# Performance work log

Measured on AMD Instinct MI355X. Metric: run time of the kernel, lower is better.

The kernel has to match this reference:

```python
import jax, jax.numpy as jnp
import numpy as np

EPS = 1e-5
D_STATE = 16
D_INNER = 2
D_CONV = 4


def batchnorm(x, g, b):
    # BatchNorm1d in training mode: biased batch statistics over the batch dim
    m = x.mean(axis=0)
    v = x.var(axis=0)
    return g * (x - m) * jax.lax.rsqrt(v + EPS) + b


def mamba(u, W_in, conv_w, conv_b, W_xproj, W_dt, b_dt, A_log, D, W_out):
    # u: [B, L, 1] (d_model=1, d_inner=2, d_state=16, dt_rank=1)
    Bsz, L, _ = u.shape
    xz = jnp.einsum('bld,ed->ble', u, W_in)            # [B,L,4]
    x, z = jnp.split(xz, 2, axis=-1)                    # [B,L,2] each
    # causal depthwise conv along L
    xc = jnp.transpose(x, (0, 2, 1))                    # [B,C,L]
    xc = jax.lax.conv_general_dilated(
        xc, conv_w, (1,), [(D_CONV - 1, 0)],
        dimension_numbers=('NCH', 'OIH', 'NCH'),
        feature_group_count=D_INNER)
    x = jax.nn.silu(jnp.transpose(xc, (0, 2, 1)) + conv_b)  # [B,L,2]
    x_dbl = jnp.einsum('ble,fe->blf', x, W_xproj)       # [B,L,1+2*16]
    dt = jax.nn.softplus(jnp.einsum('blr,er->ble', x_dbl[..., :1], W_dt) + b_dt)  # [B,L,2]
    Bm = x_dbl[..., 1:1 + D_STATE]                      # [B,L,16]
    Cm = x_dbl[..., 1 + D_STATE:1 + 2 * D_STATE]        # [B,L,16]
    A = -jnp.exp(A_log)                                 # [2,16]

    def step(h, inp):
        dt_t, B_t, C_t, x_t = inp                       # [B,2],[B,16],[B,16],[B,2]
        dA = jnp.exp(dt_t[:, :, None] * A)              # [B,2,16]
        h = h * dA + dt_t[:, :, None] * B_t[:, None, :] * x_t[:, :, None]
        y = jnp.einsum('ben,bn->be', h, C_t) + D * x_t
        return h, y

    h0 = jnp.zeros((Bsz, D_INNER, D_STATE), u.dtype)
    xs = (dt.transpose(1, 0, 2), Bm.transpose(1, 0, 2),
          Cm.transpose(1, 0, 2), x.transpose(1, 0, 2))
    _, ys = jax.lax.scan(step, h0, xs)                  # [L,B,2]
    y = ys.transpose(1, 0, 2) * jax.nn.silu(z)          # [B,L,2]
    return jnp.einsum('ble,de->bld', y, W_out)          # [B,L,1]


def setup_inputs() -> dict:
    key = jax.random.key(0)
    ks = jax.random.split(key, 16)
    B = 1024
    s = 0.02
    inp = {
        'x': jax.random.normal(ks[0], (B, 1775), jnp.float32),
        'W1': jax.random.normal(ks[1], (2048, 1775), jnp.float32) * s,
        'g1': jnp.ones((2048,), jnp.float32),
        'b1': jnp.zeros((2048,), jnp.float32),
        'W_in': jax.random.normal(ks[2], (2 * D_INNER, 1), jnp.float32) * s,
        'conv_w': jax.random.normal(ks[3], (D_INNER, 1, D_CONV), jnp.float32) * 0.2,
        'conv_b': jnp.zeros((D_INNER,), jnp.float32),
        'W_xproj': jax.random.normal(ks[4], (1 + 2 * D_STATE, D_INNER), jnp.float32) * 0.2,
        'W_dt': jax.random.normal(ks[5], (D_INNER, 1), jnp.float32) * 0.2,
        'b_dt': jax.random.normal(ks[6], (D_INNER,), jnp.float32) * 0.2,
        'A_log': jnp.tile(jnp.log(jnp.arange(1, D_STATE + 1, dtype=jnp.float32)), (D_INNER, 1)),
        'D': jnp.ones((D_INNER,), jnp.float32),
        'W_out': jax.random.normal(ks[7], (1, D_INNER), jnp.float32) * 0.2,
        'W2': jax.random.normal(ks[8], (512, 2048), jnp.float32) * s,
        'g2': jnp.ones((512,), jnp.float32),
        'b2': jnp.zeros((512,), jnp.float32),
        'W3': jax.random.normal(ks[9], (256, 512), jnp.float32) * s,
    }
    return inp


def reference(x, W1, g1, b1, W_in, conv_w, conv_b, W_xproj, W_dt, b_dt,
              A_log, D, W_out, W2, g2, b2, W3):
    h = batchnorm(x @ W1.T, g1, b1)                     # [B,2048]
    h = mamba(h[:, :, None], W_in, conv_w, conv_b, W_xproj, W_dt, b_dt,
              A_log, D, W_out)[:, :, 0]                 # [B,2048]
    h = jax.nn.relu(batchnorm(h @ W2.T, g2, b2))        # [B,512]
    return h @ W3.T                                     # [B,256]
```

## Files before the change

kernel.cpp:

```cpp
#include <hip/hip_runtime.h>
#include <math.h>

#define SEQL 2048
#define BATCH 1024
#define CHUNK 128
#define NCH 16

typedef _Float16 f16x8 __attribute__((ext_vector_type(8)));
typedef _Float16 f16x4 __attribute__((ext_vector_type(4)));
typedef _Float16 h2 __attribute__((ext_vector_type(2)));
typedef float f32x4 __attribute__((ext_vector_type(4)));

__device__ inline unsigned short f2h(float f) {
    _Float16 h = (_Float16)f;
    return *reinterpret_cast<unsigned short*>(&h);
}
__device__ inline float packh2(float a, float b) {
    return __uint_as_float((unsigned)f2h(a) | ((unsigned)f2h(b) << 16));
}
__device__ inline float hext(float packed, int sh) {
    const unsigned short s = (unsigned short)(__float_as_uint(packed) >> sh);
    _Float16 h = *reinterpret_cast<const _Float16*>(&s);
    return (float)h;
}

__device__ inline void gl2lds16(const void* g, void* l) {
    __builtin_amdgcn_global_load_lds(
        (const __attribute__((address_space(1))) unsigned int*)g,
        (__attribute__((address_space(3))) unsigned int*)l, 16, 0, 0);
}

template<int CTRL>
__device__ inline float dppadd(float v) {
    const int p = __builtin_amdgcn_update_dpp(0, __float_as_int(v), CTRL, 0xF, 0xF, true);
    return v + __int_as_float(p);
}

__global__ __launch_bounds__(256) void cvt_all(
    const float* __restrict__ x, const float* __restrict__ W1,
    const float* __restrict__ W2, const float* __restrict__ W3,
    _Float16* __restrict__ xh, _Float16* __restrict__ w1h,
    _Float16* __restrict__ w2h, _Float16* __restrict__ w3h)
{
    const int bid = blockIdx.x;
    if (bid < 3072) {
        const float* src; _Float16* dst;
        if (bid < 1024) { src = x + (size_t)bid * 1775;           dst = xh  + (size_t)bid * 1792; }
        else            { src = W1 + (size_t)(bid - 1024) * 1775; dst = w1h + (size_t)(bid - 1024) * 1792; }
        f16x4* dst4 = reinterpret_cast<f16x4*>(dst);
        for (int i = threadIdx.x; i < 448; i += 256) {
            const int k = i * 4;
            float4 v = {0.f, 0.f, 0.f, 0.f};
            if (k + 3 < 1775) v = *reinterpret_cast<const float4*>(&src[k]);
            else {
                if (k     < 1775) v.x = src[k];
                if (k + 1 < 1775) v.y = src[k + 1];
                if (k + 2 < 1775) v.z = src[k + 2];
            }
            f16x4 o; o[0] = (_Float16)v.x; o[1] = (_Float16)v.y; o[2] = (_Float16)v.z; o[3] = (_Float16)v.w;
            dst4[i] = o;
        }
    } else {
        const float* src; _Float16* dst; int nvec;
        if (bid < 3584) { const int r = bid - 3072; src = W2 + (size_t)r * 2048; dst = w2h + (size_t)r * 2048; nvec = 512; }
        else            { const int r = bid - 3584; src = W3 + (size_t)r * 512;  dst = w3h + (size_t)r * 512;  nvec = 128; }
        f16x4* dst4 = reinterpret_cast<f16x4*>(dst);
        for (int i = threadIdx.x; i < nvec; i += 256) {
            const float4 v = reinterpret_cast<const float4*>(src)[i];
            f16x4 o; o[0] = (_Float16)v.x; o[1] = (_Float16)v.y; o[2] = (_Float16)v.z; o[3] = (_Float16)v.w;
            dst4[i] = o;
        }
    }
}

__global__ __launch_bounds__(256) void cvt_bnrelu(
    const float* __restrict__ P0, const float* __restrict__ P1,
    const float* __restrict__ sc, const float* __restrict__ tc,
    _Float16* __restrict__ h3)
{
    const int row = blockIdx.x * 2 + (threadIdx.x >> 7);
    const int i = threadIdx.x & 127;
    const float4 p0 = reinterpret_cast<const float4*>(P0 + (size_t)row * 512)[i];
    const float4 p1 = reinterpret_cast<const float4*>(P1 + (size_t)row * 512)[i];
    const float4 sv = reinterpret_cast<const float4*>(sc)[i];
    const float4 tv = reinterpret_cast<const float4*>(tc)[i];
    f16x4 o;
    o[0] = (_Float16)fmaxf(fmaf(sv.x, p0.x + p1.x, tv.x), 0.f);
    o[1] = (_Float16)fmaxf(fmaf(sv.y, p0.y + p1.y, tv.y), 0.f);
    o[2] = (_Float16)fmaxf(fmaf(sv.z, p0.z + p1.z, tv.z), 0.f);
    o[3] = (_Float16)fmaxf(fmaf(sv.w, p0.w + p1.w, tv.w), 0.f);
    reinterpret_cast<f16x4*>(h3 + (size_t)row * 512)[i] = o;
}

__global__ __launch_bounds__(256) void gemm_f16(
    const _Float16* __restrict__ A, const _Float16* __restrict__ B,
    float* __restrict__ C, int ldc, int Kp, int ksteps, size_t coff,
    float* __restrict__ bnp, int bn_ld)
{
    __shared__ __attribute__((aligned(16))) _Float16 sA[64 * 64];
    __shared__ __attribute__((aligned(16))) _Float16 sB[64 * 64];

    const int tid = threadIdx.x;
    const int wave = tid >> 6;
    const int lane = tid & 63;
    const int m0 = blockIdx.y * 64;
    const int n0 = blockIdx.x * 64;
    C += (size_t)blockIdx.z * coff;

    const int srow = tid >> 3;
    const int pslot = tid & 7;
    const int gslot = pslot ^ (srow & 7);
    const size_t gk0 = (size_t)blockIdx.z * ksteps * 64 + gslot * 8;
    const _Float16* gA0 = A + (size_t)(m0 + srow) * Kp + gk0;
    const _Float16* gA1 = A + (size_t)(m0 + 32 + srow) * Kp + gk0;
    const _Float16* gB0 = B + (size_t)(n0 + srow) * Kp + gk0;
    const _Float16* gB1 = B + (size_t)(n0 + 32 + srow) * Kp + gk0;
    const int wdst = wave * 512;

    const int wr = wave >> 1, wc = wave & 1;
    const int li = lane & 15, gq = lane >> 4;
    const int p0s = (gq    ) ^ (li & 7);
    const int p1s = (gq + 4) ^ (li & 7);

    f32x4 acc[2][2];
    #pragma unroll
    for (int i = 0; i < 2; ++i)
        #pragma unroll
        for (int j = 0; j < 2; ++j)
            #pragma unroll
            for (int v = 0; v < 4; ++v) acc[i][j][v] = 0.f;

    for (int kt = 0; kt < ksteps; ++kt) {
        const size_t go = (size_t)kt * 64;
        gl2lds16(gA0 + go, &sA[wdst]);
        gl2lds16(gA1 + go, &sA[2048 + wdst]);
        gl2lds16(gB0 + go, &sB[wdst]);
        gl2lds16(gB1 + go, &sB[2048 + wdst]);
        __syncthreads();

        f16x8 af[2][2], bg[2][2];
        #pragma unroll
        for (int mi = 0; mi < 2; ++mi) {
            const int rb = (wr * 32 + mi * 16 + li) * 64;
            af[mi][0] = *(const f16x8*)&sA[rb + p0s * 8];
            af[mi][1] = *(const f16x8*)&sA[rb + p1s * 8];
        }
        #pragma unroll
        for (int ni = 0; ni < 2; ++ni) {
            const int rb = (wc * 32 + ni * 16 + li) * 64;
            bg[ni][0] = *(const f16x8*)&sB[rb + p0s * 8];
            bg[ni][1] = *(const f16x8*)&sB[rb + p1s * 8];
        }
        #pragma unroll
        for (int mi = 0; mi < 2; ++mi)
            #pragma unroll
            for (int ni = 0; ni < 2; ++ni) {
                acc[mi][ni] = __builtin_amdgcn_mfma_f32_16x16x32_f16(af[mi][0], bg[ni][0], acc[mi][ni], 0, 0, 0);
                acc[mi][ni] = __builtin_amdgcn_mfma_f32_16x16x32_f16(af[mi][1], bg[ni][1], acc[mi][ni], 0, 0, 0);
            }
        __syncthreads();
    }

    #pragma unroll
    for (int mi = 0; mi < 2; ++mi)
        #pragma unroll
        for (int ni = 0; ni < 2; ++ni) {
            const int col = n0 + wc * 32 + ni * 16 + li;
            #pragma unroll
            for (int i = 0; i < 4; ++i) {
                const int row = m0 + wr * 32 + mi * 16 + gq * 4 + i;
                C[(size_t)row * ldc + col] = acc[mi][ni][i];
            }
        }

    if (bnp) {
        #pragma unroll
        for (int ni = 0; ni < 2; ++ni) {
            float ps = 0.f, pq = 0.f;
            #pragma unroll
            for (int mi = 0; mi < 2; ++mi)
                #pragma unroll
                for (int i = 0; i < 4; ++i) {
                    const float v = acc[mi][ni][i];
                    ps += v; pq += v * v;
                }
            ps += __shfl_xor(ps, 16); ps += __shfl_xor(ps, 32);
            pq += __shfl_xor(pq, 16); pq += __shfl_xor(pq, 32);
            if (gq == 0) {
                const int col = n0 + wc * 32 + ni * 16 + li;
                const int grp = blockIdx.y * 2 + wr;
                bnp[(size_t)(grp * 2    ) * bn_ld + col] = ps;
                bnp[(size_t)(grp * 2 + 1) * bn_ld + col] = pq;
            }
        }
    }
}

__global__ __launch_bounds__(256) void bn_part(
    const float* __restrict__ X, const float* __restrict__ X2,
    int rows_per, int ld, float* __restrict__ part)
{
    __shared__ float rs[4][64], rq[4][64];
    const int tid = threadIdx.x;
    const int c = tid & 63, rg4 = tid >> 6;
    const int col = blockIdx.x * 64 + c;
    const int r0 = blockIdx.y * rows_per;
    float sum = 0.f, sq = 0.f;
    for (int r = rg4; r < rows_per; r += 4) {
        const size_t idx = (size_t)(r0 + r) * ld + col;
        float v = X[idx];
        if (X2) v += X2[idx];
        sum += v; sq += v * v;
    }
    rs[rg4][c] = sum; rq[rg4][c] = sq;
    __syncthreads();
    if (rg4 == 0) {
        sum = rs[0][c] + rs[1][c] + rs[2][c] + rs[3][c];
        sq  = rq[0][c] + rq[1][c] + rq[2][c] + rq[3][c];
        part[((size_t)blockIdx.y * 2    ) * ld + col] = sum;
        part[((size_t)blockIdx.y * 2 + 1) * ld + col] = sq;
    }
}

__global__ __launch_bounds__(256) void bn_fin(
    const float* __restrict__ part, int RG, int ld, float inv_rows,
    const float* __restrict__ g, const float* __restrict__ b,
    float* __restrict__ s, float* __restrict__ t)
{
    const int col = blockIdx.x * 256 + threadIdx.x;
    if (col >= ld) return;
    float sum = 0.f, sq = 0.f;
    for (int z = 0; z < RG; ++z) {
        sum += part[((size_t)z * 2    ) * ld + col];
        sq  += part[((size_t)z * 2 + 1) * ld + col];
    }
    const float mean = sum * inv_rows;
    const float var = fmaxf(sq * inv_rows - mean * mean, 0.f);
    const float rstd = 1.0f / sqrtf(var + 1e-5f);
    const float sv = g[col] * rstd;
    s[col] = sv;
    t[col] = b[col] - mean * sv;
}

__global__ __launch_bounds__(512, 8) void mamba_scan7(
    const float* __restrict__ Y, _Float16* __restrict__ a2,
    const float* __restrict__ s1, const float* __restrict__ t1,
    const float* __restrict__ Win, const float* __restrict__ convw,
    const float* __restrict__ convb, const float* __restrict__ Wx,
    const float* __restrict__ Wdt, const float* __restrict__ bdt,
    const float* __restrict__ Alog, const float* __restrict__ Dp,
    const float* __restrict__ Wout)
{
    __shared__ __align__(16) float4 pk[SEQL];
    __shared__ float Ps[NCH][32];
    __shared__ float Ss[NCH][32];
    __shared__ float Hin[NCH][32];

    const int tid = threadIdx.x;
    const int row = blockIdx.x;
    const float* yrow = Y + (size_t)row * SEQL;
    _Float16* a2row = a2 + (size_t)row * SEQL;

    {
        const int l0 = tid * 4;
        float4 ym = {0.f,0.f,0.f,0.f}, sm = {0.f,0.f,0.f,0.f}, tm = {0.f,0.f,0.f,0.f};
        if (tid > 0) {
            ym = *reinterpret_cast<const float4*>(&yrow[l0 - 4]);
            sm = *reinterpret_cast<const float4*>(&s1[l0 - 4]);
            tm = *reinterpret_cast<const float4*>(&t1[l0 - 4]);
        }
        const float4 y0 = *reinterpret_cast<const float4*>(&yrow[l0]);
        const float4 s0 = *reinterpret_cast<const float4*>(&s1[l0]);
        const float4 t0 = *reinterpret_cast<const float4*>(&t1[l0]);

        float ua[8];
        ua[0] = fmaf(sm.x, ym.x, tm.x);
        ua[1] = fmaf(sm.y, ym.y, tm.y);
        ua[2] = fmaf(sm.z, ym.z, tm.z);
        ua[3] = fmaf(sm.w, ym.w, tm.w);
        ua[4] = fmaf(s0.x, y0.x, t0.x);
        ua[5] = fmaf(s0.y, y0.y, t0.y);
        ua[6] = fmaf(s0.z, y0.z, t0.z);
        ua[7] = fmaf(s0.w, y0.w, t0.w);

        const float wi0 = Win[0], wi1 = Win[1];
        const float wz0 = Win[2], wz1 = Win[3];
        const float wo0 = Wout[0], wo1 = Wout[1];
        const float cw00 = convw[0], cw01 = convw[1], cw02 = convw[2], cw03 = convw[3];
        const float cw10 = convw[4], cw11 = convw[5], cw12 = convw[6], cw13 = convw[7];
        const float cb0 = convb[0], cb1 = convb[1];
        const float wx00 = Wx[0], wx01 = Wx[1];
        const float wdt0 = Wdt[0], wdt1 = Wdt[1];
        const float bdt0 = bdt[0], bdt1 = bdt[1];

        #pragma unroll
        for (int j = 0; j < 4; ++j) {
            const float u0 = ua[j + 4], um1 = ua[j + 3], um2 = ua[j + 2], um3 = ua[j + 1];
            const float c0 = fmaf(wi0, cw00 * um3 + cw01 * um2 + cw02 * um1 + cw03 * u0, cb0);
            const float c1 = fmaf(wi1, cw10 * um3 + cw11 * um2 + cw12 * um1 + cw13 * u0, cb1);
            const float xs0 = c0 / (1.f + __expf(-c0));
            const float xs1 = c1 / (1.f + __expf(-c1));
            const float d0 = xs0 * wx00 + xs1 * wx01;
            const float dt0 = __logf(1.f + __expf(fmaf(d0, wdt0, bdt0)));
            const float dt1 = __logf(1.f + __expf(fmaf(d0, wdt1, bdt1)));
            const float z0 = u0 * wz0, z1 = u0 * wz1;
            const float g0 = (z0 / (1.f + __expf(-z0))) * wo0;
            const float g1 = (z1 / (1.f + __expf(-z1))) * wo1;
            float4 rec;
            rec.x = dt0; rec.y = dt1;
            rec.z = packh2(xs0, xs1);
            rec.w = packh2(g0, g1);
            pk[l0 + j] = rec;
        }
    }
    __syncthreads();

    const int c  = tid >> 5;
    const int l5 = tid & 31;
    const int e  = l5 >> 4;
    const int n  = l5 & 15;
    const int base = c * CHUNK;
    const int esh = e * 16;

    const float Aen2 = -__expf(Alog[e * 16 + n]) * 1.44269504f;
    h2 wxB2, wxC2;
    wxB2[0] = (_Float16)Wx[(1 + n) * 2 + 0];
    wxB2[1] = (_Float16)Wx[(1 + n) * 2 + 1];
    wxC2[0] = (_Float16)Wx[(17 + n) * 2 + 0];
    wxC2[1] = (_Float16)Wx[(17 + n) * 2 + 1];

    {
        float h = 0.f, p = 1.f;
        for (int i0 = 0; i0 < CHUNK; i0 += 8) {
            #pragma unroll
            for (int j = 0; j < 8; ++j) {
                const float4 v = pk[base + i0 + j];
                const float dte = e ? v.y : v.x;
                const h2 xs2 = __builtin_bit_cast(h2, v.z);
                const float Bn = __builtin_amdgcn_fdot2(xs2, wxB2, 0.f, false);
                const float xe = hext(v.z, esh);
                const float dA = __builtin_amdgcn_exp2f(dte * Aen2);
                h = fmaf(h, dA, dte * xe * Bn);
                p *= dA;
            }
        }
        Ps[c][l5] = p;
        Ss[c][l5] = h;
    }
    __syncthreads();

    if (tid < 32) {
        float H = 0.f;
        #pragma unroll
        for (int cc = 0; cc < NCH; ++cc) {
            Hin[cc][tid] = H;
            H = fmaf(Ps[cc][tid], H, Ss[cc][tid]);
        }
    }
    __syncthreads();

    {
        const float De = Dp[e];
        float h = Hin[c][l5];
        for (int i0 = 0; i0 < CHUNK; i0 += 8) {
            float qs[8];
            #pragma unroll
            for (int j = 0; j < 8; ++j) {
                const float4 v = pk[base + i0 + j];
                const float dte = e ? v.y : v.x;
                const h2 xs2 = __builtin_bit_cast(h2, v.z);
                const float Bn = __builtin_amdgcn_fdot2(xs2, wxB2, 0.f, false);
                const float Cn = __builtin_amdgcn_fdot2(xs2, wxC2, 0.f, false);
                const float xe = hext(v.z, esh);
                const float ge = hext(v.w, esh);
                const float dA = __builtin_amdgcn_exp2f(dte * Aen2);
                h = fmaf(h, dA, dte * xe * Bn);
                float q = h * Cn;
                q = dppadd<0xB1>(q);
                q = dppadd<0x4E>(q);
                q = dppadd<0x141>(q);
                q = dppadd<0x140>(q);
                q = fmaf(De, xe, q) * ge;
                q = dppadd<0x142>(q);
                qs[j] = q;
            }
            if (l5 == 16) {
                float4 st;
                st.x = __builtin_bit_cast(float, __builtin_amdgcn_cvt_pkrtz(qs[0], qs[1]));
                st.y = __builtin_bit_cast(float, __builtin_amdgcn_cvt_pkrtz(qs[2], qs[3]));
                st.z = __builtin_bit_cast(float, __builtin_amdgcn_cvt_pkrtz(qs[4], qs[5]));
                st.w = __builtin_bit_cast(float, __builtin_amdgcn_cvt_pkrtz(qs[6], qs[7]));
                *reinterpret_cast<float4*>(&a2row[base + i0]) = st;
            }
        }
    }
}

extern "C" void kernel_launch(void* const* d_in, const int* in_sizes, int n_in,
                              void* d_out, int out_size, void* d_ws, size_t ws_size,
                              hipStream_t stream)
{
    const float* x     = (const float*)d_in[0];
    const float* W1    = (const float*)d_in[1];
    const float* g1    = (const float*)d_in[2];
    const float* b1    = (const float*)d_in[3];
    const float* Win   = (const float*)d_in[4];
    const float* convw = (const float*)d_in[5];
    const float* convb = (const float*)d_in[6];
    const float* Wx    = (const float*)d_in[7];
    const float* Wdt   = (const float*)d_in[8];
    const float* bdt   = (const float*)d_in[9];
    const float* Alog  = (const float*)d_in[10];
    const float* Dp    = (const float*)d_in[11];
    const float* Wout  = (const float*)d_in[12];
    const float* W2    = (const float*)d_in[13];
    const float* g2    = (const float*)d_in[14];
    const float* b2    = (const float*)d_in[15];
    const float* W3    = (const float*)d_in[16];

    unsigned char* base = (unsigned char*)d_ws;
    float* C1 = (float*)(base + 0);
    float* P0 = (float*)(base + 8388608);
    float* P1 = (float*)(base + 10485760);
    float* s1 = (float*)(base + 12582912);
    float* t1 = (float*)(base + 12591104);
    float* s2 = (float*)(base + 12599296);
    float* t2 = (float*)(base + 12601344);
    float* bnp = (float*)(base + 12615680);
    _Float16* a2  = (_Float16*)(base + 13172736);
    _Float16* xh  = (_Float16*)(base + 17367040);
    _Float16* w1h = (_Float16*)(base + 21037056);
    _Float16* w2h = (_Float16*)(base + 28377088);
    _Float16* w3h = (_Float16*)(base + 30474240);
    _Float16* h3h = (_Float16*)(base + 30736384);

    cvt_all<<<3840, 256, 0, stream>>>(x, W1, W2, W3, xh, w1h, w2h, w3h);

    gemm_f16<<<dim3(32, 16, 1), 256, 0, stream>>>(
        xh, w1h, C1, 2048, 1792, 28, 0, bnp, 2048);

    bn_fin<<<8, 256, 0, stream>>>(bnp, 32, 2048, 1.0f / 1024.f, g1, b1, s1, t1);

    mamba_scan7<<<1024, 512, 0, stream>>>(C1, a2, s1, t1, Win, convw, convb,
                                          Wx, Wdt, bdt, Alog, Dp, Wout);

    gemm_f16<<<dim3(8, 16, 2), 256, 0, stream>>>(
        a2, w2h, P0, 512, 2048, 16, (size_t)1024 * 512, nullptr, 0);

    bn_part<<<dim3(8, 16), 256, 0, stream>>>(P0, P1, 64, 512, bnp);
    bn_fin<<<2, 256, 0, stream>>>(bnp, 16, 512, 1.0f / 1024.f, g2, b2, s2, t2);

    cvt_bnrelu<<<512, 256, 0, stream>>>(P0, P1, s2, t2, h3h);

    gemm_f16<<<dim3(4, 16, 1), 256, 0, stream>>>(
        h3h, w3h, (float*)d_out, 256, 512, 8, 0, nullptr, 0);
}
```

Baseline: 148.4 us.

## Remap scan threads so each lane holds both channels over halved chunks

Each thread now owns one state index n for both inner channels. Chunks shrink from 128 to 64 steps, and there are 32 chunks instead of 16. The inner channels are merged in-thread before the cross-lane reduction, which drops one DPP step. The D*x*gate term is computed with an fp16 dot instead of per-lane. The change aims to halve the serial chunk length and share the pk loads and B/C dot products across both channels. In exchange it doubles per-thread exp work, lengthens the serial carry pass to 32 chunks, and computes the D term in fp16 precision.

```diff
diff --git a/kernel.cpp b/kernel.cpp
--- a/kernel.cpp
+++ b/kernel.cpp
@@ -3,8 +3,8 @@
 
 #define SEQL 2048
 #define BATCH 1024
-#define CHUNK 128
-#define NCH 16
+#define CHUNK 64
+#define NCH 32
 
 typedef _Float16 f16x8 __attribute__((ext_vector_type(8)));
 typedef _Float16 f16x4 __attribute__((ext_vector_type(4)));
@@ -242,7 +242,7 @@
     t[col] = b[col] - mean * sv;
 }
 
-__global__ __launch_bounds__(512, 8) void mamba_scan7(
+__global__ __launch_bounds__(512, 8) void mamba_scan8(
     const float* __restrict__ Y, _Float16* __restrict__ a2,
     const float* __restrict__ s1, const float* __restrict__ t1,
     const float* __restrict__ Win, const float* __restrict__ convw,
@@ -252,9 +252,8 @@
     const float* __restrict__ Wout)
 {
     __shared__ __align__(16) float4 pk[SEQL];
-    __shared__ float Ps[NCH][32];
-    __shared__ float Ss[NCH][32];
-    __shared__ float Hin[NCH][32];
+    __shared__ float Pa[2][NCH][16];
+    __shared__ float Sa[2][NCH][16];
 
     const int tid = threadIdx.x;
     const int row = blockIdx.x;
@@ -315,14 +314,12 @@
     }
     __syncthreads();
 
-    const int c  = tid >> 5;
-    const int l5 = tid & 31;
-    const int e  = l5 >> 4;
-    const int n  = l5 & 15;
-    const int base = c * CHUNK;
-    const int esh = e * 16;
-
-    const float Aen2 = -__expf(Alog[e * 16 + n]) * 1.44269504f;
+    const int ch = tid >> 4;
+    const int n  = tid & 15;
+    const int base = ch * CHUNK;
+
+    const float A0 = -__expf(Alog[n])      * 1.44269504f;
+    const float A1 = -__expf(Alog[16 + n]) * 1.44269504f;
     h2 wxB2, wxC2;
     wxB2[0] = (_Float16)Wx[(1 + n) * 2 + 0];
     wxB2[1] = (_Float16)Wx[(1 + n) * 2 + 1];
@@ -330,61 +327,71 @@
     wxC2[1] = (_Float16)Wx[(17 + n) * 2 + 1];
 
     {
-        float h = 0.f, p = 1.f;
+        float h0 = 0.f, h1 = 0.f, p0 = 1.f, p1 = 1.f;
         for (int i0 = 0; i0 < CHUNK; i0 += 8) {
             #pragma unroll
             for (int j = 0; j < 8; ++j) {
                 const float4 v = pk[base + i0 + j];
-                const float dte = e ? v.y : v.x;
                 const h2 xs2 = __builtin_bit_cast(h2, v.z);
                 const float Bn = __builtin_amdgcn_fdot2(xs2, wxB2, 0.f, false);
-                const float xe = hext(v.z, esh);
-                const float dA = __builtin_amdgcn_exp2f(dte * Aen2);
-                h = fmaf(h, dA, dte * xe * Bn);
-                p *= dA;
-            }
-        }
-        Ps[c][l5] = p;
-        Ss[c][l5] = h;
+                const float xs0 = hext(v.z, 0), xs1 = hext(v.z, 16);
+                const float dA0 = __builtin_amdgcn_exp2f(v.x * A0);
+                const float dA1 = __builtin_amdgcn_exp2f(v.y * A1);
+                h0 = fmaf(h0, dA0, (v.x * xs0) * Bn);
+                h1 = fmaf(h1, dA1, (v.y * xs1) * Bn);
+                p0 *= dA0; p1 *= dA1;
+            }
+        }
+        Pa[0][ch][n] = p0; Pa[1][ch][n] = p1;
+        Sa[0][ch][n] = h0; Sa[1][ch][n] = h1;
     }
     __syncthreads();
 
     if (tid < 32) {
+        const int e = tid >> 4, nn = tid & 15;
         float H = 0.f;
         #pragma unroll
         for (int cc = 0; cc < NCH; ++cc) {
-            Hin[cc][tid] = H;
-            H = fmaf(Ps[cc][tid], H, Ss[cc][tid]);
+            const float Pv = Pa[e][cc][nn];
+            const float Sv = Sa[e][cc][nn];
+            Sa[e][cc][nn] = H;
+            H = fmaf(Pv, H, Sv);
         }
     }
     __syncthreads();
 
     {
-        const float De = Dp[e];
-        float h = Hin[c][l5];
+        h2 D2h;
+        D2h[0] = (_Float16)Dp[0];
+        D2h[1] = (_Float16)Dp[1];
+        float h0 = Sa[0][ch][n], h1 = Sa[1][ch][n];
         for (int i0 = 0; i0 < CHUNK; i0 += 8) {
             float qs[8];
             #pragma unroll
             for (int j = 0; j < 8; ++j) {
                 const float4 v = pk[base + i0 + j];
-                const float dte = e ? v.y : v.x;
                 const h2 xs2 = __builtin_bit_cast(h2, v.z);
+                const h2 gg2 = __builtin_bit_cast(h2, v.w);
                 const float Bn = __builtin_amdgcn_fdot2(xs2, wxB2, 0.f, false);
                 const float Cn = __builtin_amdgcn_fdot2(xs2, wxC2, 0.f, false);
-                const float xe = hext(v.z, esh);
-                const float ge = hext(v.w, esh);
-                const float dA = __builtin_amdgcn_exp2f(dte * Aen2);
-                h = fmaf(h, dA, dte * xe * Bn);
-                float q = h * Cn;
+                const float xs0 = hext(v.z, 0), xs1 = hext(v.z, 16);
+                const float g0 = hext(v.w, 0),  g1 = hext(v.w, 16);
+                const float dA0 = __builtin_amdgcn_exp2f(v.x * A0);
+                const float dA1 = __builtin_amdgcn_exp2f(v.y * A1);
+                h0 = fmaf(h0, dA0, (v.x * xs0) * Bn);
+                h1 = fmaf(h1, dA1, (v.y * xs1) * Bn);
+                float t = h0 * g0;
+                t = fmaf(h1, g1, t);
+                float q = t * Cn;
                 q = dppadd<0xB1>(q);
                 q = dppadd<0x4E>(q);
                 q = dppadd<0x141>(q);
                 q = dppadd<0x140>(q);
-                q = fmaf(De, xe, q) * ge;
-                q = dppadd<0x142>(q);
-                qs[j] = q;
-            }
-            if (l5 == 16) {
+                const h2 dgh = D2h * gg2;
+                const float dterm = __builtin_amdgcn_fdot2(xs2, dgh, 0.f, false);
+                qs[j] = q + dterm;
+            }
+            if (n == 0) {
                 float4 st;
                 st.x = __builtin_bit_cast(float, __builtin_amdgcn_cvt_pkrtz(qs[0], qs[1]));
                 st.y = __builtin_bit_cast(float, __builtin_amdgcn_cvt_pkrtz(qs[2], qs[3]));
@@ -441,7 +448,7 @@
 
     bn_fin<<<8, 256, 0, stream>>>(bnp, 32, 2048, 1.0f / 1024.f, g1, b1, s1, t1);
 
-    mamba_scan7<<<1024, 512, 0, stream>>>(C1, a2, s1, t1, Win, convw, convb,
+    mamba_scan8<<<1024, 512, 0, stream>>>(C1, a2, s1, t1, Win, convw, convb,
                                           Wx, Wdt, bdt, Alog, Dp, Wout);
 
     gemm_f16<<<dim3(8, 16, 2), 256, 0, stream>>>(
```

Measured after the change: 127.3 us. 14.2% less time.
